# Kernel optimization log

Hardware: AMD Instinct MI355X
Metric: run time of the kernel (lower is better)

The kernel has to match this reference:

```python
import jax, jax.numpy as jnp
import numpy as np

G = 16  # self.group
K = 3   # unfold/fold kernel size


def setup_inputs() -> dict:
    key = jax.random.key(0)
    feature = jax.random.normal(key, (2, 128, 192, 192), dtype=jnp.float32)
    return {"feature": feature}


def reference(feature):
    B, C, H, W = feature.shape
    Cg = C // G
    Hm, Wm = H - K + 1, W - K + 1
    L = Hm * Wm

    # --- nn.Unfold(kernel_size=3), all groups at once ---
    # patches[b, c, k, y, x] with k = ki*3 + kj (channel-major flat = c*9 + k)
    slices = [feature[:, :, ki:ki + Hm, kj:kj + Wm] for ki in range(K) for kj in range(K)]
    patches = jnp.stack(slices, axis=2)                 # [B, C, 9, Hm, Wm]
    # per-group series flat dim is Cg*9 (order cg*9+k); chunk(9) -> reshape [9, Cg]
    motif = patches.reshape(B, G, Cg * 9, L).reshape(B, G, 9, Cg, L)  # [B,G,9,Cg,L]

    # --- cdist + diag=inf + argmin (squared distances: same argmin as p=2) ---
    gram = jnp.einsum('bgjcl,bgjdl->bgjcd', motif, motif)   # [B,G,9,Cg,Cg]
    sq = jnp.einsum('bgjcl,bgjcl->bgjc', motif, motif)      # [B,G,9,Cg]
    d2 = sq[..., :, None] + sq[..., None, :] - 2.0 * gram
    eye = jnp.eye(Cg, dtype=bool)
    d2 = jnp.where(eye, jnp.inf, d2)
    nn_idx = jnp.argmin(d2, axis=-1)                        # [B,G,9,Cg] int

    # --- torch.unique loop overwrites motif_new: only the LAST (max) unique
    # index and its count survive ---
    u_max = jnp.max(nn_idx, axis=-1)                        # [B,G,9]
    c_max = jnp.sum(nn_idx == u_max[..., None], axis=-1).astype(feature.dtype)  # [B,G,9]

    motif_nn = jnp.take_along_axis(motif, u_max[..., None, None], axis=3)  # [B,G,9,1,L]
    # float '//' in torch is floor division
    term = jnp.floor(motif * motif_nn * c_max[..., None, None] / Cg)
    # l == 0 branch drops the '+ motif' term
    batch_mask = (jnp.arange(B) != 0).astype(feature.dtype).reshape(B, 1, 1, 1, 1)
    out_ser = motif * batch_mask + term                     # [B,G,9,Cg,L]

    # --- nn.Fold: input layout reinterpreted as (channel, kernel) flat = c*9+k ---
    ser2 = out_ser.reshape(B, G, 9 * Cg, L).reshape(B, G, Cg, 9, Hm, Wm)
    out = jnp.zeros((B, G, Cg, H, W), feature.dtype)
    for k in range(K * K):
        ki, kj = k // K, k % K
        out = out.at[:, :, :, ki:ki + Hm, kj:kj + Wm].add(ser2[:, :, :, k])
    return out.reshape(B, C, H, W)
```

## Files before the change

### kernel.cpp

```cpp
#include <hip/hip_runtime.h>
#include <hip/hip_bf16.h>
#include <math.h>

#define BB 2
#define CC 128
#define GG 16
#define CG 8
#define HH 192
#define WW 192
#define HM 190
#define WM 190
#define LL (HM * WM)
#define HWSZ (HH * WW)
#define NTRIPLE (BB * GG * 9)
#define SPLIT 6
#define ROWS_PER_SLICE 32

typedef float float4a __attribute__((ext_vector_type(4), aligned(4)));
typedef float float4v __attribute__((ext_vector_type(4)));

__device__ float g_part[NTRIPLE * SPLIT * 36];
__device__ int g_rel[BB * GG * 72];
__device__ float g_scl[BB * GG * 72];

__global__ __launch_bounds__(256) void phase1a_kernel(
    const float* __restrict__ feat) {
  const int B = blockIdx.x;
  const int xcd = B & 7;
  const int slot = B >> 3;
  const int unit = xcd * 4 + slot / 54;
  const int r = slot % 54;
  const int j = r / 6;
  const int sl = r % 6;
  const int b = unit >> 4;
  const int g = unit & 15;

  const float* base[8];
#pragma unroll
  for (int d = 0; d < 8; ++d) {
    const int f = j * 8 + d;
    const int c = f / 9;
    const int k = f % 9;
    const int ki = k / 3, kj = k % 3;
    base[d] = feat + (size_t)(b * CC + g * CG + c) * HWSZ + ki * WW + kj;
  }

  float acc[36];
#pragma unroll
  for (int i = 0; i < 36; ++i) acc[i] = 0.0f;

  const int y0 = sl * ROWS_PER_SLICE;
  const int y1 = (y0 + ROWS_PER_SLICE < HM) ? y0 + ROWS_PER_SLICE : HM;
  const int ng = (y1 - y0) * 48;

  for (int gi = (int)threadIdx.x; gi < ng; gi += 256) {
    const int y = y0 + gi / 48;
    const int xg = gi % 48;
    const bool tail = (xg == 47);
    const int xL = tail ? 186 : xg * 4;
    const int ro = y * WW + xL;
    float4a v[8];
#pragma unroll
    for (int d = 0; d < 8; ++d) v[d] = *(const float4a*)(base[d] + ro);
    if (tail) {
#pragma unroll
      for (int d = 0; d < 8; ++d) {
        v[d].x = 0.0f;
        v[d].y = 0.0f;
      }
    }
#pragma unroll
    for (int d = 0; d < 8; ++d)
      acc[d] += v[d].x * v[d].x + v[d].y * v[d].y + v[d].z * v[d].z +
                v[d].w * v[d].w;
    int p = 8;
#pragma unroll
    for (int c = 0; c < 8; ++c)
#pragma unroll
      for (int d = c + 1; d < 8; ++d) {
        acc[p] += v[c].x * v[d].x + v[c].y * v[d].y + v[c].z * v[d].z +
                  v[c].w * v[d].w;
        ++p;
      }
  }

  __shared__ float red[36 * 4];
  const int lane = threadIdx.x & 63;
  const int wave = threadIdx.x >> 6;
#pragma unroll
  for (int i = 0; i < 36; ++i) {
    float v = acc[i];
    for (int o = 32; o > 0; o >>= 1) v += __shfl_down(v, o, 64);
    if (lane == 0) red[i * 4 + wave] = v;
  }
  __syncthreads();
  if (threadIdx.x < 36) {
    const int i = threadIdx.x;
    const int tri = unit * 9 + j;
    g_part[(tri * SPLIT + sl) * 36 + i] =
        red[i * 4] + red[i * 4 + 1] + red[i * 4 + 2] + red[i * 4 + 3];
  }
}

__global__ __launch_bounds__(64) void phase1b_kernel() {
  const int tri = blockIdx.x * 64 + (int)threadIdx.x;
  if (tri >= NTRIPLE) return;
  const int b = tri / (GG * 9);
  const int rem = tri % (GG * 9);
  const int g = rem / 9;
  const int j = rem % 9;

  float tot[36];
#pragma unroll
  for (int i = 0; i < 36; ++i) tot[i] = 0.0f;
  for (int s = 0; s < SPLIT; ++s)
#pragma unroll
    for (int i = 0; i < 36; ++i) tot[i] += g_part[(tri * SPLIT + s) * 36 + i];

  float sq[8], gm[8][8];
#pragma unroll
  for (int i = 0; i < 8; ++i) sq[i] = tot[i];
  {
    int p = 8;
    for (int c = 0; c < 8; ++c)
      for (int d = c + 1; d < 8; ++d) {
        gm[c][d] = tot[p];
        gm[d][c] = tot[p];
        ++p;
      }
  }
  int nn[8];
  for (int c = 0; c < 8; ++c) {
    float best = INFINITY;
    int bi = 0;
    for (int d = 0; d < 8; ++d) {
      if (d == c) continue;
      const float d2 = sq[c] + sq[d] - 2.0f * gm[c][d];
      if (d2 < best) {
        best = d2;
        bi = d;
      }
    }
    nn[c] = bi;
  }
  int um = 0;
  for (int c = 0; c < 8; ++c) um = um > nn[c] ? um : nn[c];
  int cnt = 0;
  for (int c = 0; c < 8; ++c) cnt += (nn[c] == um) ? 1 : 0;

  const float sc = (float)cnt * 0.125f;
  const int fn = j * 8 + um;
  const int cn = fn / 9;
  const int kn = fn % 9;
  const int kin = kn / 3, kjn = kn % 3;
  for (int d = 0; d < 8; ++d) {
    const int f = j * 8 + d;
    const int cl = f / 9;
    const int k = f % 9;
    const int ki = k / 3, kj = k % 3;
    const int rel = (cn - cl) * HWSZ + (kin - ki) * WW + (kjn - kj);
    const int tix = (b * GG + g) * 72 + f;
    g_rel[tix] = rel;
    g_scl[tix] = sc;
  }
}

__global__ __launch_bounds__(256) void phase2_main_kernel(
    const float* __restrict__ feat, float* __restrict__ out) {
  const int B = blockIdx.x;
  const int xcd = B & 7;
  const int slot = B >> 3;
  const int unit = xcd * 4 + slot / 144;
  const int r = slot % 144;
  const int cl = r / 18;
  const int blk = r % 18;
  const int plane = unit * 8 + cl;

  const int tbase = unit * 72 + cl * 9;
  int rel[9];
  float scl[9];
#pragma unroll
  for (int k = 0; k < 9; ++k) {
    rel[k] = g_rel[tbase + k];
    scl[k] = g_scl[tbase + k];
  }

  const float* pb = feat + (size_t)plane * HWSZ;
  float* ob = out + (size_t)plane * HWSZ;
  const bool b1 = (unit >= GG);
  const int i0 = blk * 2048 + (int)threadIdx.x * 4;

#pragma unroll
  for (int gidx = 0; gidx < 2; ++gidx) {
    const int inner = i0 + gidx * 1024;
    const int h = inner / WW;
    const int w0 = inner % WW;
    if (h >= 2 && h < HM && w0 >= 4 && w0 < 188) {
      const float* p = pb + inner;
      const float4v v = *(const float4v*)p;
      float4v acc = {0.0f, 0.0f, 0.0f, 0.0f};
#pragma unroll
      for (int k = 0; k < 9; ++k) {
        const float4a n = *(const float4a*)(p + rel[k]);
        const float s = scl[k];
        acc.x += floorf(v.x * n.x * s);
        acc.y += floorf(v.y * n.y * s);
        acc.z += floorf(v.z * n.z * s);
        acc.w += floorf(v.w * n.w * s);
      }
      if (b1) {
        acc.x += 9.0f * v.x;
        acc.y += 9.0f * v.y;
        acc.z += 9.0f * v.z;
        acc.w += 9.0f * v.w;
      }
      *(float4v*)(ob + inner) = acc;
    }
  }
}

__global__ __launch_bounds__(256) void phase2_edge_kernel(
    const float* __restrict__ feat, float* __restrict__ out) {
  const int gid = blockIdx.x * 256 + (int)threadIdx.x;
  const int plane = gid / 2272;
  const int ei = gid % 2272;
  int h, w;
  if (ei < 768) {
    const int r = ei / WW;
    h = (r < 2) ? r : r + 188;
    w = ei % WW;
  } else {
    const int e2 = ei - 768;
    h = 2 + (e2 >> 3);
    const int w8 = e2 & 7;
    w = (w8 < 4) ? w8 : w8 + 184;
  }
  const int g = (plane % CC) >> 3;
  const int cl = (plane % CC) & 7;
  const int tbase = ((plane / CC) * GG + g) * 72 + cl * 9;

  int rel[9];
  float scl[9];
#pragma unroll
  for (int k = 0; k < 9; ++k) {
    rel[k] = g_rel[tbase + k];
    scl[k] = g_scl[tbase + k];
  }

  const int idx = plane * HWSZ + h * WW + w;
  const float* p = feat + idx;
  const float v = *p;
  float acc = 0.0f;
  int nv = 0;
#pragma unroll
  for (int k = 0; k < 9; ++k) {
    const int ki = k / 3, kj = k % 3;
    const int y = h - ki, x = w - kj;
    const bool valid = ((unsigned)y < (unsigned)HM) & ((unsigned)x < (unsigned)WM);
    const int o = valid ? rel[k] : 0;
    const float n = p[o];
    const float fl = floorf(v * n * scl[k]);
    acc += valid ? fl : 0.0f;
    nv += valid ? 1 : 0;
  }
  if (plane >= CC) acc += (float)nv * v;
  out[idx] = acc;
}

extern "C" void kernel_launch(void* const* d_in, const int* in_sizes, int n_in,
                              void* d_out, int out_size, void* d_ws,
                              size_t ws_size, hipStream_t stream) {
  const float* feat = (const float*)d_in[0];
  float* out = (float*)d_out;
  (void)d_ws;
  (void)ws_size;

  phase1a_kernel<<<NTRIPLE * SPLIT, 256, 0, stream>>>(feat);
  phase1b_kernel<<<(NTRIPLE + 63) / 64, 64, 0, stream>>>();

  phase2_main_kernel<<<BB * CC * 18, 256, 0, stream>>>(feat, out);
  phase2_edge_kernel<<<2272, 256, 0, stream>>>(feat, out);
}
```

Baseline: 137.0 us.

## Stage input rows in LDS for Gram-matrix phase instead of global float4 loads

```diff
diff --git a/kernel.cpp b/kernel.cpp
--- a/kernel.cpp
+++ b/kernel.cpp
@@ -14,7 +14,9 @@
 #define HWSZ (HH * WW)
 #define NTRIPLE (BB * GG * 9)
 #define SPLIT 6
-#define ROWS_PER_SLICE 32
+#define RPS 32
+#define STG_ROWS 34
+#define STG_STRIDE (STG_ROWS * WW)
 
 typedef float float4a __attribute__((ext_vector_type(4), aligned(4)));
 typedef float float4v __attribute__((ext_vector_type(4)));
@@ -35,56 +37,56 @@
   const int b = unit >> 4;
   const int g = unit & 15;
 
-  const float* base[8];
+  const int cA = (8 * j) / 9;
+  const int cB = (8 * j + 7) / 9;
+  const int y0 = sl * RPS;
+  const int y1 = (y0 + RPS < HM) ? y0 + RPS : HM;
+  const int nstage = ((y1 + 2 < HH) ? y1 + 2 : HH) - y0;
+
+  __shared__ __attribute__((aligned(16))) float lds[2 * STG_STRIDE];
+  __shared__ float red[36 * 4];
+
+  const int nch = (cB != cA) ? 2 : 1;
+  for (int ch = 0; ch < nch; ++ch) {
+    const int c = ch ? cB : cA;
+    const float4v* src = (const float4v*)(feat +
+        (size_t)(b * CC + g * CG + c) * HWSZ + (size_t)y0 * WW);
+    float4v* dst = (float4v*)(lds + ch * STG_STRIDE);
+    const int nvec = nstage * (WW / 4);
+    for (int i = (int)threadIdx.x; i < nvec; i += 256) dst[i] = src[i];
+  }
+  __syncthreads();
+
+  int ldb[8];
 #pragma unroll
   for (int d = 0; d < 8; ++d) {
     const int f = j * 8 + d;
     const int c = f / 9;
     const int k = f % 9;
-    const int ki = k / 3, kj = k % 3;
-    base[d] = feat + (size_t)(b * CC + g * CG + c) * HWSZ + ki * WW + kj;
+    ldb[d] = (c == cA ? 0 : STG_STRIDE) + (k / 3) * WW + (k % 3);
   }
 
   float acc[36];
 #pragma unroll
   for (int i = 0; i < 36; ++i) acc[i] = 0.0f;
 
-  const int y0 = sl * ROWS_PER_SLICE;
-  const int y1 = (y0 + ROWS_PER_SLICE < HM) ? y0 + ROWS_PER_SLICE : HM;
-  const int ng = (y1 - y0) * 48;
-
-  for (int gi = (int)threadIdx.x; gi < ng; gi += 256) {
-    const int y = y0 + gi / 48;
-    const int xg = gi % 48;
-    const bool tail = (xg == 47);
-    const int xL = tail ? 186 : xg * 4;
-    const int ro = y * WW + xL;
-    float4a v[8];
-#pragma unroll
-    for (int d = 0; d < 8; ++d) v[d] = *(const float4a*)(base[d] + ro);
-    if (tail) {
-#pragma unroll
-      for (int d = 0; d < 8; ++d) {
-        v[d].x = 0.0f;
-        v[d].y = 0.0f;
-      }
-    }
-#pragma unroll
-    for (int d = 0; d < 8; ++d)
-      acc[d] += v[d].x * v[d].x + v[d].y * v[d].y + v[d].z * v[d].z +
-                v[d].w * v[d].w;
+  const int npix = (y1 - y0) * WM;
+  for (int l = (int)threadIdx.x; l < npix; l += 256) {
+    const int y = l / WM;
+    const int x = l - y * WM;
+    const int o = y * WW + x;
+    float v[8];
+#pragma unroll
+    for (int d = 0; d < 8; ++d) v[d] = lds[ldb[d] + o];
+#pragma unroll
+    for (int d = 0; d < 8; ++d) acc[d] += v[d] * v[d];
     int p = 8;
 #pragma unroll
     for (int c = 0; c < 8; ++c)
 #pragma unroll
-      for (int d = c + 1; d < 8; ++d) {
-        acc[p] += v[c].x * v[d].x + v[c].y * v[d].y + v[c].z * v[d].z +
-                  v[c].w * v[d].w;
-        ++p;
-      }
-  }
-
-  __shared__ float red[36 * 4];
+      for (int d = c + 1; d < 8; ++d) acc[p++] += v[c] * v[d];
+  }
+
   const int lane = threadIdx.x & 63;
   const int wave = threadIdx.x >> 6;
 #pragma unroll
```

Result: slower. 153.3 us (+11.9%).

## Reuse shared channel rows across shifted unfold taps in gram phase

Applied to the files above, without the earlier changes.

```diff
diff --git a/kernel.cpp b/kernel.cpp
--- a/kernel.cpp
+++ b/kernel.cpp
@@ -18,12 +18,100 @@
 
 typedef float float4a __attribute__((ext_vector_type(4), aligned(4)));
 typedef float float4v __attribute__((ext_vector_type(4)));
+typedef float float2v __attribute__((ext_vector_type(2), aligned(8)));
 
 __device__ float g_part[NTRIPLE * SPLIT * 36];
 __device__ int g_rel[BB * GG * 72];
 __device__ float g_scl[BB * GG * 72];
 
-__global__ __launch_bounds__(256) void phase1a_kernel(
+template <int J>
+__device__ __forceinline__ void gram_slice(const float* __restrict__ pA,
+                                           const float* __restrict__ pB,
+                                           int y0, int rows, int tid,
+                                           float acc[36]) {
+  constexpr int CA = (8 * J) / 9;
+  constexpr int CB = (8 * J + 7) / 9;
+  constexpr int NCH = (CB > CA) ? 2 : 1;
+
+  const int npair = rows * 23;
+  for (int q = tid; q < npair; q += 256) {
+    const int y = y0 + q / 23;
+    const int x0 = (q % 23) * 8;
+    const int ro = y * WW + x0;
+
+    float w[NCH][3][10];
+#pragma unroll
+    for (int ci = 0; ci < NCH; ++ci) {
+      const float* pc = ci ? pB : pA;
+#pragma unroll
+      for (int ki = 0; ki < 3; ++ki) {
+        const float4v a = *(const float4v*)(pc + ro + ki * WW);
+        const float4v bq = *(const float4v*)(pc + ro + ki * WW + 4);
+        const float2v cq = *(const float2v*)(pc + ro + ki * WW + 8);
+        w[ci][ki][0] = a.x; w[ci][ki][1] = a.y;
+        w[ci][ki][2] = a.z; w[ci][ki][3] = a.w;
+        w[ci][ki][4] = bq.x; w[ci][ki][5] = bq.y;
+        w[ci][ki][6] = bq.z; w[ci][ki][7] = bq.w;
+        w[ci][ki][8] = cq.x; w[ci][ki][9] = cq.y;
+      }
+    }
+#pragma unroll
+    for (int d = 0; d < 8; ++d) {
+      const int f = 8 * J + d;
+      const int ci = f / 9 - CA;
+      const int k = f % 9;
+      const int ki = k / 3, kj = k % 3;
+      float s = 0.0f;
+#pragma unroll
+      for (int e = 0; e < 8; ++e) s += w[ci][ki][kj + e] * w[ci][ki][kj + e];
+      acc[d] += s;
+    }
+    int p = 8;
+#pragma unroll
+    for (int c = 0; c < 8; ++c) {
+      const int f1 = 8 * J + c;
+      const int ci1 = f1 / 9 - CA;
+      const int k1 = f1 % 9;
+      const int ki1 = k1 / 3, kj1 = k1 % 3;
+#pragma unroll
+      for (int d = c + 1; d < 8; ++d) {
+        const int f2 = 8 * J + d;
+        const int ci2 = f2 / 9 - CA;
+        const int k2 = f2 % 9;
+        const int ki2 = k2 / 3, kj2 = k2 % 3;
+        float s = 0.0f;
+#pragma unroll
+        for (int e = 0; e < 8; ++e)
+          s += w[ci1][ki1][kj1 + e] * w[ci2][ki2][kj2 + e];
+        acc[p++] += s;
+      }
+    }
+  }
+
+  const int ncl = rows * 6;
+  for (int t = tid; t < ncl; t += 256) {
+    const int y = y0 + t / 6;
+    const int x = 184 + t % 6;
+    float v[8];
+#pragma unroll
+    for (int d = 0; d < 8; ++d) {
+      const int f = 8 * J + d;
+      const int ci = f / 9 - CA;
+      const int k = f % 9;
+      const int ki = k / 3, kj = k % 3;
+      v[d] = (ci ? pB : pA)[(y + ki) * WW + x + kj];
+    }
+#pragma unroll
+    for (int d = 0; d < 8; ++d) acc[d] += v[d] * v[d];
+    int p = 8;
+#pragma unroll
+    for (int c = 0; c < 8; ++c)
+#pragma unroll
+      for (int d = c + 1; d < 8; ++d) acc[p++] += v[c] * v[d];
+  }
+}
+
+__global__ __launch_bounds__(256, 4) void phase1a_kernel(
     const float* __restrict__ feat) {
   const int B = blockIdx.x;
   const int xcd = B & 7;
@@ -35,58 +123,35 @@
   const int b = unit >> 4;
   const int g = unit & 15;
 
-  const float* base[8];
-#pragma unroll
-  for (int d = 0; d < 8; ++d) {
-    const int f = j * 8 + d;
-    const int c = f / 9;
-    const int k = f % 9;
-    const int ki = k / 3, kj = k % 3;
-    base[d] = feat + (size_t)(b * CC + g * CG + c) * HWSZ + ki * WW + kj;
-  }
-
-  float acc[36];
-#pragma unroll
-  for (int i = 0; i < 36; ++i) acc[i] = 0.0f;
+  const int cA = (8 * j) / 9;
+  const int cB = (8 * j + 7) / 9;
+  const float* pA = feat + (size_t)(b * CC + g * CG + cA) * HWSZ;
+  const float* pB = feat + (size_t)(b * CC + g * CG + cB) * HWSZ;
 
   const int y0 = sl * ROWS_PER_SLICE;
   const int y1 = (y0 + ROWS_PER_SLICE < HM) ? y0 + ROWS_PER_SLICE : HM;
-  const int ng = (y1 - y0) * 48;
-
-  for (int gi = (int)threadIdx.x; gi < ng; gi += 256) {
-    const int y = y0 + gi / 48;
-    const int xg = gi % 48;
-    const bool tail = (xg == 47);
-    const int xL = tail ? 186 : xg * 4;
-    const int ro = y * WW + xL;
-    float4a v[8];
-#pragma unroll
-    for (int d = 0; d < 8; ++d) v[d] = *(const float4a*)(base[d] + ro);
-    if (tail) {
-#pragma unroll
-      for (int d = 0; d < 8; ++d) {
-        v[d].x = 0.0f;
-        v[d].y = 0.0f;
-      }
-    }
-#pragma unroll
-    for (int d = 0; d < 8; ++d)
-      acc[d] += v[d].x * v[d].x + v[d].y * v[d].y + v[d].z * v[d].z +
-                v[d].w * v[d].w;
-    int p = 8;
-#pragma unroll
-    for (int c = 0; c < 8; ++c)
-#pragma unroll
-      for (int d = c + 1; d < 8; ++d) {
-        acc[p] += v[c].x * v[d].x + v[c].y * v[d].y + v[c].z * v[d].z +
-                  v[c].w * v[d].w;
-        ++p;
-      }
+  const int rows = y1 - y0;
+  const int tid = (int)threadIdx.x;
+
+  float acc[36];
+#pragma unroll
+  for (int i = 0; i < 36; ++i) acc[i] = 0.0f;
+
+  switch (j) {
+    case 0: gram_slice<0>(pA, pB, y0, rows, tid, acc); break;
+    case 1: gram_slice<1>(pA, pB, y0, rows, tid, acc); break;
+    case 2: gram_slice<2>(pA, pB, y0, rows, tid, acc); break;
+    case 3: gram_slice<3>(pA, pB, y0, rows, tid, acc); break;
+    case 4: gram_slice<4>(pA, pB, y0, rows, tid, acc); break;
+    case 5: gram_slice<5>(pA, pB, y0, rows, tid, acc); break;
+    case 6: gram_slice<6>(pA, pB, y0, rows, tid, acc); break;
+    case 7: gram_slice<7>(pA, pB, y0, rows, tid, acc); break;
+    default: gram_slice<8>(pA, pB, y0, rows, tid, acc); break;
   }
 
   __shared__ float red[36 * 4];
-  const int lane = threadIdx.x & 63;
-  const int wave = threadIdx.x >> 6;
+  const int lane = tid & 63;
+  const int wave = tid >> 6;
 #pragma unroll
   for (int i = 0; i < 36; ++i) {
     float v = acc[i];
@@ -94,8 +159,8 @@
     if (lane == 0) red[i * 4 + wave] = v;
   }
   __syncthreads();
-  if (threadIdx.x < 36) {
-    const int i = threadIdx.x;
+  if (tid < 36) {
+    const int i = tid;
     const int tri = unit * 9 + j;
     g_part[(tri * SPLIT + sl) * 36 + i] =
         red[i * 4] + red[i * 4 + 1] + red[i * 4 + 2] + red[i * 4 + 3];
```

After: 199.9 us. 45.9% more time.
